# Kernel tuning notes

Hardware: AMD Instinct MI355X
Metric: run time of the kernel (lower is better)

The kernel has to match this reference:

```python
import jax, jax.numpy as jnp
import numpy as np

N, E, F_IN, H, MH, C, G = 100000, 3200000, 128, 32, 64, 10, 64

def _seg_sum(data, ids, num):
    return jax.ops.segment_sum(data, ids, num_segments=num)

def gcn_conv(x, row, col, ew, W, b, n):
    # PyG GCNConv: linear first, then self-loops + symmetric edge-weight norm + scatter-add
    h = x @ W  # [N, H]
    loop = jnp.arange(n)
    r = jnp.concatenate([row, loop])
    c = jnp.concatenate([col, loop])
    w = jnp.concatenate([ew, jnp.ones((n,), dtype=ew.dtype)])
    deg = _seg_sum(w, c, n)
    dinv = jnp.where(deg > 0, jax.lax.rsqrt(deg), 0.0)
    norm = dinv[r] * w * dinv[c]  # [E+N]
    out = _seg_sum(norm[:, None] * h[r], c, n)  # scatter to targets
    return out + b

def setup_inputs():
    key = jax.random.key(0)
    ks = jax.random.split(key, 16)
    inp = {
        "x": jax.random.normal(ks[0], (N, F_IN), dtype=jnp.float32),
        "edge_index": jax.random.randint(ks[1], (2, E), 0, N, dtype=jnp.int64),
        "edge_weight": jax.random.uniform(ks[2], (E,), dtype=jnp.float32),
        "batch": jnp.sort(jax.random.randint(ks[3], (N,), 0, G, dtype=jnp.int64)),
    }
    def lin(k, i, o):
        s = 1.0 / np.sqrt(i)
        k1, k2 = jax.random.split(k)
        return (jax.random.uniform(k1, (i, o), minval=-s, maxval=s, dtype=jnp.float32),
                jax.random.uniform(k2, (o,), minval=-s, maxval=s, dtype=jnp.float32))
    inp["W1"], inp["b1"] = lin(ks[4], F_IN, H)
    inp["W2"], inp["b2"] = lin(ks[5], H, H)
    inp["W3"], inp["b3"] = lin(ks[6], H, H)
    inp["Wm0"], inp["bm0"] = lin(ks[7], H, MH)
    inp["Wm1"], inp["bm1"] = lin(ks[8], MH, MH)
    inp["Wout"], inp["bout"] = lin(ks[9], MH, C)
    return inp

def reference(x, edge_index, edge_weight, batch, W1, b1, W2, b2, W3, b3, Wm0, bm0, Wm1, bm1, Wout, bout):
    row, col = edge_index[0], edge_index[1]
    h = jax.nn.relu(gcn_conv(x, row, col, edge_weight, W1, b1, N))
    h = jax.nn.relu(gcn_conv(h, row, col, edge_weight, W2, b2, N))
    h = gcn_conv(h, row, col, edge_weight, W3, b3, N)
    # global mean pool over graphs
    sums = _seg_sum(h, batch, G)
    counts = _seg_sum(jnp.ones((N,), dtype=h.dtype), batch, G)
    g = sums / jnp.maximum(counts, 1.0)[:, None]
    # dropout p=0.5 is identity at inference (training=False)
    g = jax.nn.relu(g @ Wm0 + bm0)
    g = jax.nn.relu(g @ Wm1 + bm1)
    return g @ Wout + bout
```

## Files before the change

kernel.cpp:

```cpp
#include <hip/hip_runtime.h>

#define NN 100000
#define NE 3200000
#define FIN 128
#define HID 32
#define MH  64
#define NC  10
#define NG  64
#define NBKT 782
#define NBLK 512
#define EPB  (NE / NBLK)
#define SCANL (NBKT * NBLK)
#define SRCMASK 0x1FFFF
#define BCAP 5120

typedef float floatx2 __attribute__((ext_vector_type(2)));

__global__ __launch_bounds__(1024)
void hist_bkt(const int* __restrict__ ei, int* __restrict__ cnt2) {
    __shared__ int h[NBKT];
    int tid = threadIdx.x, blk = blockIdx.x;
    for (int b = tid; b < NBKT; b += 1024) h[b] = 0;
    __syncthreads();
    int base = blk * EPB;
    for (int i = tid; i < EPB; i += 1024)
        atomicAdd(&h[ei[NE + base + i] >> 7], 1);
    __syncthreads();
    for (int b = tid; b < NBKT; b += 1024) cnt2[b * NBLK + blk] = h[b];
}

__global__ void scan_block(const int* __restrict__ in, int* __restrict__ out,
                           int* __restrict__ bsum, int n) {
    __shared__ int lds[256];
    int tid = threadIdx.x;
    int base = blockIdx.x * 1024 + tid * 4;
    int v0 = 0, v1 = 0, v2 = 0, v3 = 0;
    if (base + 0 < n) v0 = in[base + 0];
    if (base + 1 < n) v1 = in[base + 1];
    if (base + 2 < n) v2 = in[base + 2];
    if (base + 3 < n) v3 = in[base + 3];
    int s = v0 + v1 + v2 + v3;
    lds[tid] = s;
    __syncthreads();
    for (int off = 1; off < 256; off <<= 1) {
        int val = (tid >= off) ? lds[tid - off] : 0;
        __syncthreads();
        lds[tid] += val;
        __syncthreads();
    }
    int excl = lds[tid] - s;
    if (tid == 255) bsum[blockIdx.x] = lds[255];
    if (base + 0 < n) out[base + 0] = excl;
    if (base + 1 < n) out[base + 1] = excl + v0;
    if (base + 2 < n) out[base + 2] = excl + v0 + v1;
    if (base + 3 < n) out[base + 3] = excl + v0 + v1 + v2;
}

__global__ void scan_top(int* __restrict__ bsum, int nb, float* __restrict__ sc) {
    int lane = threadIdx.x;
    for (int i = lane; i < NG * HID + NG; i += 64) sc[i] = 0.0f;
    int carry = 0;
    for (int base = 0; base < nb; base += 64) {
        int i = base + lane;
        int orig = (i < nb) ? bsum[i] : 0;
        int v = orig;
#pragma unroll
        for (int off = 1; off < 64; off <<= 1) {
            int t = __shfl_up(v, off, 64);
            if (lane >= off) v += t;
        }
        if (i < nb) bsum[i] = carry + v - orig;
        carry += __shfl(v, 63, 64);
    }
}

__global__ __launch_bounds__(1024)
void scatter_bkt(const int* __restrict__ ei, const float* __restrict__ ew,
                 const int* __restrict__ cnt2, const int* __restrict__ scanned,
                 const int* __restrict__ bsum, int2* __restrict__ tre) {
    __shared__ int2 pay[EPB];
    __shared__ int scur[NBKT];
    __shared__ int hexc[NBKT];
    __shared__ int gbase[NBKT];
    int tid = threadIdx.x, blk = blockIdx.x;
    int myh = 0;
    if (tid < NBKT) {
        int idx = tid * NBLK + blk;
        myh = cnt2[idx];
        gbase[tid] = scanned[idx] + bsum[idx >> 10];
        scur[tid] = myh;
    }
    __syncthreads();
    for (int off = 1; off < NBKT; off <<= 1) {
        int v = (tid < NBKT && tid >= off) ? scur[tid - off] : 0;
        __syncthreads();
        if (tid < NBKT) scur[tid] += v;
        __syncthreads();
    }
    if (tid < NBKT) { int ex = scur[tid] - myh; hexc[tid] = ex; scur[tid] = ex; }
    __syncthreads();
    int base = blk * EPB;
    for (int i = tid; i < EPB; i += 1024) {
        int e = base + i;
        int c = ei[NE + e];
        int r = ei[e];
        unsigned int wb = __float_as_uint(ew[e]);
        int b = c >> 7;
        int j = atomicAdd(&scur[b], 1);
        pay[j] = make_int2(r | ((c & 127) << 17) | ((b & 0xFF) << 24),
                           (int)((wb & ~3u) | ((unsigned)b >> 8)));
    }
    __syncthreads();
    for (int j = tid; j < EPB; j += 1024) {
        int2 q = pay[j];
        int b = (int)((((unsigned)q.y & 3u) << 8) | (((unsigned)q.x >> 24) & 0xFFu));
        int pos = gbase[b] + (j - hexc[b]);
        tre[pos] = make_int2(q.x & 0x00FFFFFF, q.y & ~3);
    }
}

__global__ __launch_bounds__(512)
void sort_k(const int2* __restrict__ tre, const int* __restrict__ scanned,
            const int* __restrict__ bsum, unsigned int* __restrict__ srn4,
            int* __restrict__ rowptr, float* __restrict__ dinv) {
    __shared__ int2 ed[BCAP];
    __shared__ int h[128];
    __shared__ float dw[128];
    __shared__ int cur[128];
    int b = blockIdx.x, tid = threadIdx.x;
    int base = scanned[b * NBLK] + bsum[(b * NBLK) >> 10];
    int end = (b == NBKT - 1)
                  ? NE
                  : scanned[(b + 1) * NBLK] + bsum[((b + 1) * NBLK) >> 10];
    int n = end - base;
    bool staged = (n <= BCAP);
    if (tid < 128) { h[tid] = 0; dw[tid] = 0.f; }
    __syncthreads();
    for (int i = tid; i < n; i += 512) {
        int2 q = tre[base + i];
        if (staged) ed[i] = q;
        int key = (q.x >> 17) & 127;
        atomicAdd(&h[key], 1);
        atomicAdd(&dw[key], __int_as_float(q.y));
    }
    __syncthreads();
    if (tid < 64) {
        int lane = tid;
        int carry = 0;
#pragma unroll
        for (int c = 0; c < 2; ++c) {
            int idx = c * 64 + lane;
            int hv = h[idx];
            int v = hv;
#pragma unroll
            for (int off = 1; off < 64; off <<= 1) {
                int t = __shfl_up(v, off, 64);
                if (lane >= off) v += t;
            }
            cur[idx] = base + carry + v - hv;
            int node = b * 128 + idx;
            if (node < NN) {
                rowptr[node] = base + carry + v;
                dinv[node] = rsqrtf(1.0f + dw[idx]);
            }
            carry += __shfl(v, 63, 64);
        }
    }
    __syncthreads();
    for (int i = tid; i < n; i += 512) {
        int2 q = staged ? ed[i] : tre[base + i];
        int key = (q.x >> 17) & 127;
        int pos = atomicAdd(&cur[key], 1);
        unsigned int wb = (unsigned)q.y;
        wb += 0x7FFFu + ((wb >> 16) & 1u);
        srn4[pos] = (unsigned)(q.x & SRCMASK) | (((wb >> 16) & 0x7FFFu) << 17);
    }
}

template <int IN_DIM, bool RELU_IN>
__global__ __launch_bounds__(256)
void linear_k(const float* __restrict__ in, const float* __restrict__ W,
              const float* __restrict__ dinv, unsigned int* __restrict__ tmp8) {
    constexpr int J4 = IN_DIM / 4;
    constexpr int XSS = J4 + 1;
    __shared__ float4 xs[64 * XSS];
    __shared__ float4 wp[IN_DIM * 8];
    int tid = threadIdx.x;
    for (int idx = tid; idx < IN_DIM * 8; idx += 256) {
        int j = idx >> 3, kg = idx & 7;
        const float* wr = W + j * 32 + kg * 4;
        wp[idx] = make_float4(wr[0], wr[1], wr[2], wr[3]);
    }
    int rbase = blockIdx.x * 64;
    const float4* in4 = (const float4*)in;
    for (int idx = tid; idx < 64 * J4; idx += 256) {
        int row = idx / J4, j4 = idx % J4;
        int grow = rbase + row;
        float4 v = (grow < NN) ? in4[(size_t)grow * J4 + j4]
                               : make_float4(0.f, 0.f, 0.f, 0.f);
        if (RELU_IN) {
            v.x = fmaxf(v.x, 0.f); v.y = fmaxf(v.y, 0.f);
            v.z = fmaxf(v.z, 0.f); v.w = fmaxf(v.w, 0.f);
        }
        xs[row * XSS + j4] = v;
    }
    __syncthreads();
    int kg = tid & 7;
    int rp = tid >> 3;
    int r0 = rbase + 2 * rp;
    if (r0 >= NN) return;
    const float4* x0 = &xs[(2 * rp) * XSS];
    const float4* x1 = &xs[(2 * rp + 1) * XSS];
    float a00 = 0, a01 = 0, a02 = 0, a03 = 0;
    float a10 = 0, a11 = 0, a12 = 0, a13 = 0;
#pragma unroll
    for (int j4 = 0; j4 < J4; ++j4) {
        float4 v0 = x0[j4], v1 = x1[j4];
        const float4* wj = &wp[j4 * 4 * 8 + kg];
        float4 w0 = wj[0], w1 = wj[8], w2 = wj[16], w3 = wj[24];
#define LSTEP(VX0, VX1, W4) \
        a00 = fmaf(VX0, W4.x, a00); a01 = fmaf(VX0, W4.y, a01); \
        a02 = fmaf(VX0, W4.z, a02); a03 = fmaf(VX0, W4.w, a03); \
        a10 = fmaf(VX1, W4.x, a10); a11 = fmaf(VX1, W4.y, a11); \
        a12 = fmaf(VX1, W4.z, a12); a13 = fmaf(VX1, W4.w, a13);
        LSTEP(v0.x, v1.x, w0)
        LSTEP(v0.y, v1.y, w1)
        LSTEP(v0.z, v1.z, w2)
        LSTEP(v0.w, v1.w, w3)
#undef LSTEP
    }
    float d0 = dinv[r0], d1 = dinv[r0 + 1];
    a00 *= d0; a01 *= d0; a02 *= d0; a03 *= d0;
    a10 *= d1; a11 *= d1; a12 *= d1; a13 *= d1;
    int q0 = __builtin_amdgcn_cvt_pk_fp8_f32(a00, a01, 0, false);
    q0 = __builtin_amdgcn_cvt_pk_fp8_f32(a02, a03, q0, true);
    int q1 = __builtin_amdgcn_cvt_pk_fp8_f32(a10, a11, 0, false);
    q1 = __builtin_amdgcn_cvt_pk_fp8_f32(a12, a13, q1, true);
    tmp8[r0 * 8 + kg] = (unsigned int)q0;
    tmp8[(r0 + 1) * 8 + kg] = (unsigned int)q1;
}

struct AccR { floatx2 r0, r1, r2, r3, r4, r5, r6, r7; };

#define ACC8(A0,A1,A2,A3,A4,A5,A6,A7, U, W) { \
    floatx2 lo_, hi_; \
    lo_ = __builtin_amdgcn_cvt_pk_f32_fp8(U.x, false); \
    hi_ = __builtin_amdgcn_cvt_pk_f32_fp8(U.x, true); \
    A0 += lo_ * W; A1 += hi_ * W; \
    lo_ = __builtin_amdgcn_cvt_pk_f32_fp8(U.y, false); \
    hi_ = __builtin_amdgcn_cvt_pk_f32_fp8(U.y, true); \
    A2 += lo_ * W; A3 += hi_ * W; \
    lo_ = __builtin_amdgcn_cvt_pk_f32_fp8(U.z, false); \
    hi_ = __builtin_amdgcn_cvt_pk_f32_fp8(U.z, true); \
    A4 += lo_ * W; A5 += hi_ * W; \
    lo_ = __builtin_amdgcn_cvt_pk_f32_fp8(U.w, false); \
    hi_ = __builtin_amdgcn_cvt_pk_f32_fp8(U.w, true); \
    A6 += lo_ * W; A7 += hi_ * W; }

__device__ __forceinline__ AccR agg_core(const unsigned int* __restrict__ srn4,
                                         const int* __restrict__ rowptr,
                                         const unsigned int* __restrict__ tmp8,
                                         int nid, int s, unsigned int cb) {
    const char* t8 = (const char*)tmp8;
    int end = rowptr[nid];
    int start = (nid == 0) ? 0 : rowptr[nid - 1];
    floatx2 a0 = {0.f,0.f}, a1 = {0.f,0.f}, a2 = {0.f,0.f}, a3 = {0.f,0.f};
    floatx2 a4 = {0.f,0.f}, a5 = {0.f,0.f}, a6 = {0.f,0.f}, a7 = {0.f,0.f};
    floatx2 b0 = {0.f,0.f}, b1 = {0.f,0.f}, b2 = {0.f,0.f}, b3 = {0.f,0.f};
    floatx2 b4 = {0.f,0.f}, b5 = {0.f,0.f}, b6 = {0.f,0.f}, b7 = {0.f,0.f};
    int eM = end - 1;
    for (int e = start + s; e < end; e += 32) {
        int i1 = min(e + 8, eM);
        int i2 = min(e + 16, eM);
        int i3 = min(e + 24, eM);
        unsigned int p0 = srn4[e];
        unsigned int p1 = srn4[i1];
        unsigned int p2 = srn4[i2];
        unsigned int p3 = srn4[i3];
        uint4 u0 = *(const uint4*)(t8 + (((p0 & SRCMASK) << 5) | cb));
        uint4 u1 = *(const uint4*)(t8 + (((p1 & SRCMASK) << 5) | cb));
        uint4 u2 = *(const uint4*)(t8 + (((p2 & SRCMASK) << 5) | cb));
        uint4 u3 = *(const uint4*)(t8 + (((p3 & SRCMASK) << 5) | cb));
        float w0 = __uint_as_float((p0 >> 1) & 0x7FFF0000u);
        float w1 = (e + 8  <= eM) ? __uint_as_float((p1 >> 1) & 0x7FFF0000u) : 0.f;
        float w2 = (e + 16 <= eM) ? __uint_as_float((p2 >> 1) & 0x7FFF0000u) : 0.f;
        float w3 = (e + 24 <= eM) ? __uint_as_float((p3 >> 1) & 0x7FFF0000u) : 0.f;
        ACC8(a0,a1,a2,a3,a4,a5,a6,a7, u0, w0)
        ACC8(b0,b1,b2,b3,b4,b5,b6,b7, u1, w1)
        ACC8(a0,a1,a2,a3,a4,a5,a6,a7, u2, w2)
        ACC8(b0,b1,b2,b3,b4,b5,b6,b7, u3, w3)
    }
    a0 += b0; a1 += b1; a2 += b2; a3 += b3;
    a4 += b4; a5 += b5; a6 += b6; a7 += b7;
#define REDM(M) { \
    a0.x += __shfl_xor(a0.x, M, 64); a0.y += __shfl_xor(a0.y, M, 64); \
    a1.x += __shfl_xor(a1.x, M, 64); a1.y += __shfl_xor(a1.y, M, 64); \
    a2.x += __shfl_xor(a2.x, M, 64); a2.y += __shfl_xor(a2.y, M, 64); \
    a3.x += __shfl_xor(a3.x, M, 64); a3.y += __shfl_xor(a3.y, M, 64); \
    a4.x += __shfl_xor(a4.x, M, 64); a4.y += __shfl_xor(a4.y, M, 64); \
    a5.x += __shfl_xor(a5.x, M, 64); a5.y += __shfl_xor(a5.y, M, 64); \
    a6.x += __shfl_xor(a6.x, M, 64); a6.y += __shfl_xor(a6.y, M, 64); \
    a7.x += __shfl_xor(a7.x, M, 64); a7.y += __shfl_xor(a7.y, M, 64); }
    REDM(2) REDM(4) REDM(8)
#undef REDM
    AccR r;
    r.r0 = a0; r.r1 = a1; r.r2 = a2; r.r3 = a3;
    r.r4 = a4; r.r5 = a5; r.r6 = a6; r.r7 = a7;
    return r;
}

#define EPILOGUE16(O0,O1,O2,O3, NID, CB, D, BIAS, A, RELU) { \
    const char* t8_ = (const char*)tmp8; \
    uint4 sv_ = *(const uint4*)(t8_ + (((unsigned)(NID)) << 5) + (CB)); \
    floatx2 s0_ = __builtin_amdgcn_cvt_pk_f32_fp8(sv_.x, false); \
    floatx2 s1_ = __builtin_amdgcn_cvt_pk_f32_fp8(sv_.x, true); \
    floatx2 s2_ = __builtin_amdgcn_cvt_pk_f32_fp8(sv_.y, false); \
    floatx2 s3_ = __builtin_amdgcn_cvt_pk_f32_fp8(sv_.y, true); \
    floatx2 s4_ = __builtin_amdgcn_cvt_pk_f32_fp8(sv_.z, false); \
    floatx2 s5_ = __builtin_amdgcn_cvt_pk_f32_fp8(sv_.z, true); \
    floatx2 s6_ = __builtin_amdgcn_cvt_pk_f32_fp8(sv_.w, false); \
    floatx2 s7_ = __builtin_amdgcn_cvt_pk_f32_fp8(sv_.w, true); \
    const float4* bp_ = (const float4*)(BIAS) + 4 * c; \
    float4 bq0_ = bp_[0], bq1_ = bp_[1], bq2_ = bp_[2], bq3_ = bp_[3]; \
    O0.x = bq0_.x + (D) * (s0_.x + A.r0.x); \
    O0.y = bq0_.y + (D) * (s0_.y + A.r0.y); \
    O0.z = bq0_.z + (D) * (s1_.x + A.r1.x); \
    O0.w = bq0_.w + (D) * (s1_.y + A.r1.y); \
    O1.x = bq1_.x + (D) * (s2_.x + A.r2.x); \
    O1.y = bq1_.y + (D) * (s2_.y + A.r2.y); \
    O1.z = bq1_.z + (D) * (s3_.x + A.r3.x); \
    O1.w = bq1_.w + (D) * (s3_.y + A.r3.y); \
    O2.x = bq2_.x + (D) * (s4_.x + A.r4.x); \
    O2.y = bq2_.y + (D) * (s4_.y + A.r4.y); \
    O2.z = bq2_.z + (D) * (s5_.x + A.r5.x); \
    O2.w = bq2_.w + (D) * (s5_.y + A.r5.y); \
    O3.x = bq3_.x + (D) * (s6_.x + A.r6.x); \
    O3.y = bq3_.y + (D) * (s6_.y + A.r6.y); \
    O3.z = bq3_.z + (D) * (s7_.x + A.r7.x); \
    O3.w = bq3_.w + (D) * (s7_.y + A.r7.y); \
    if (RELU) { \
        O0.x = fmaxf(O0.x, 0.f); O0.y = fmaxf(O0.y, 0.f); \
        O0.z = fmaxf(O0.z, 0.f); O0.w = fmaxf(O0.w, 0.f); \
        O1.x = fmaxf(O1.x, 0.f); O1.y = fmaxf(O1.y, 0.f); \
        O1.z = fmaxf(O1.z, 0.f); O1.w = fmaxf(O1.w, 0.f); \
        O2.x = fmaxf(O2.x, 0.f); O2.y = fmaxf(O2.y, 0.f); \
        O2.z = fmaxf(O2.z, 0.f); O2.w = fmaxf(O2.w, 0.f); \
        O3.x = fmaxf(O3.x, 0.f); O3.y = fmaxf(O3.y, 0.f); \
        O3.z = fmaxf(O3.z, 0.f); O3.w = fmaxf(O3.w, 0.f); \
    } }

__global__ __launch_bounds__(256)
void aggregate(const unsigned int* __restrict__ srn4,
               const int* __restrict__ rowptr,
               const float* __restrict__ dinv,
               const float* __restrict__ bias,
               const unsigned int* __restrict__ tmp8,
               float* __restrict__ h) {
    int tid = threadIdx.x;
    int nid = (blockIdx.x * 256 + tid) >> 4;
    int lane = tid & 63;
    int c = lane & 1, s = (lane >> 1) & 7;
    unsigned int cb = (unsigned int)c * 16u;
    AccR A = agg_core(srn4, rowptr, tmp8, nid, s, cb);
    if ((lane & 14) == 0) {
        float d = dinv[nid];
        float4 o0, o1, o2, o3;
        EPILOGUE16(o0, o1, o2, o3, nid, cb, d, bias, A, false)
        float4* hp = (float4*)(h + (size_t)nid * HID + 16 * c);
        hp[0] = o0; hp[1] = o1; hp[2] = o2; hp[3] = o3;
    }
}

__global__ __launch_bounds__(256)
void agg_lin(const unsigned int* __restrict__ srn4,
             const int* __restrict__ rowptr,
             const float* __restrict__ dinv,
             const float* __restrict__ bias,
             const float* __restrict__ Wn,
             const unsigned int* __restrict__ tmp8,
             unsigned int* __restrict__ tmp8_out) {
    __shared__ float hrow[4][4][HID];
    __shared__ float Wt[32][36];
    int tid = threadIdx.x;
    for (int idx = tid; idx < 1024; idx += 256)
        Wt[idx & 31][idx >> 5] = Wn[idx];
    int nid = (blockIdx.x * 256 + tid) >> 4;
    int wv = tid >> 6;
    int lane = tid & 63;
    int n = (lane >> 4) & 3;
    int c = lane & 1, s = (lane >> 1) & 7;
    unsigned int cb = (unsigned int)c * 16u;
    __syncthreads();
    AccR A = agg_core(srn4, rowptr, tmp8, nid, s, cb);
    float d = dinv[nid];
    if ((lane & 14) == 0) {
        float4 o0, o1, o2, o3;
        EPILOGUE16(o0, o1, o2, o3, nid, cb, d, bias, A, true)
        float4* hp = (float4*)&hrow[wv][n][16 * c];
        hp[0] = o0; hp[1] = o1; hp[2] = o2; hp[3] = o3;
    }
    int j0 = lane & 15;
    const float4* hb = (const float4*)&hrow[wv][n][0];
    float4 h0 = hb[0], h1 = hb[1], h2 = hb[2], h3 = hb[3];
    float4 h4 = hb[4], h5 = hb[5], h6 = hb[6], h7 = hb[7];
    const float4* w0p = (const float4*)&Wt[j0][0];
    const float4* w1p = (const float4*)&Wt[j0 + 16][0];
    float y0 = 0.f, y1 = 0.f;
#define MVSTEP(K, HV) { float4 wa_ = w0p[K]; float4 wb_ = w1p[K]; \
    y0 = fmaf(HV.x, wa_.x, y0); y0 = fmaf(HV.y, wa_.y, y0); \
    y0 = fmaf(HV.z, wa_.z, y0); y0 = fmaf(HV.w, wa_.w, y0); \
    y1 = fmaf(HV.x, wb_.x, y1); y1 = fmaf(HV.y, wb_.y, y1); \
    y1 = fmaf(HV.z, wb_.z, y1); y1 = fmaf(HV.w, wb_.w, y1); }
    MVSTEP(0, h0) MVSTEP(1, h1) MVSTEP(2, h2) MVSTEP(3, h3)
    MVSTEP(4, h4) MVSTEP(5, h5) MVSTEP(6, h6) MVSTEP(7, h7)
#undef MVSTEP
    y0 *= d; y1 *= d;
    float p1 = __shfl_down(y0, 1, 64);
    float p2 = __shfl_down(y0, 2, 64);
    float p3 = __shfl_down(y0, 3, 64);
    float q1 = __shfl_down(y1, 1, 64);
    float q2 = __shfl_down(y1, 2, 64);
    float q3 = __shfl_down(y1, 3, 64);
    if ((j0 & 3) == 0) {
        int t = j0 >> 2;
        int w0 = __builtin_amdgcn_cvt_pk_fp8_f32(y0, p1, 0, false);
        w0 = __builtin_amdgcn_cvt_pk_fp8_f32(p2, p3, w0, true);
        int w1 = __builtin_amdgcn_cvt_pk_fp8_f32(y1, q1, 0, false);
        w1 = __builtin_amdgcn_cvt_pk_fp8_f32(q2, q3, w1, true);
        tmp8_out[nid * 8 + t] = (unsigned int)w0;
        tmp8_out[nid * 8 + 4 + t] = (unsigned int)w1;
    }
}

__global__ void pool_k(const float* __restrict__ h, const int* __restrict__ batch,
                       float* __restrict__ sums, float* __restrict__ counts) {
    int t = blockIdx.x * 256 + threadIdx.x;
    int chunk = t >> 5, k = t & 31;
    int n0 = chunk * 32;
    if (n0 >= NN) return;
    int n1 = min(n0 + 32, NN);
    int g = batch[n0];
    float acc = 0.f, cacc = 0.f;
    for (int i = n0; i < n1; ++i) {
        int gi = batch[i];
        if (gi != g) {
            atomicAdd(&sums[g * HID + k], acc);
            if (k == 0) atomicAdd(&counts[g], cacc);
            g = gi; acc = 0.f; cacc = 0.f;
        }
        acc += h[(size_t)i * HID + k];
        cacc += 1.f;
    }
    atomicAdd(&sums[g * HID + k], acc);
    if (k == 0) atomicAdd(&counts[g], cacc);
}

__global__ __launch_bounds__(64)
void mlp_k(const float* __restrict__ sums, const float* __restrict__ counts,
           const float* __restrict__ Wm0, const float* __restrict__ bm0,
           const float* __restrict__ Wm1, const float* __restrict__ bm1,
           const float* __restrict__ Wout, const float* __restrict__ bout,
           float* __restrict__ out) {
    __shared__ float g0[HID];
    __shared__ float g1[MH];
    __shared__ float g2[MH];
    int g = blockIdx.x;
    int k = threadIdx.x;
    if (k < HID) g0[k] = sums[g * HID + k] / fmaxf(counts[g], 1.0f);
    __syncthreads();
    float acc = bm0[k];
#pragma unroll
    for (int j = 0; j < HID; ++j) acc = fmaf(g0[j], Wm0[j * MH + k], acc);
    g1[k] = fmaxf(acc, 0.f);
    __syncthreads();
    float acc2 = bm1[k];
#pragma unroll
    for (int j = 0; j < MH; ++j) acc2 = fmaf(g1[j], Wm1[j * MH + k], acc2);
    g2[k] = fmaxf(acc2, 0.f);
    __syncthreads();
    if (k < NC) {
        float acc3 = bout[k];
#pragma unroll
        for (int j = 0; j < MH; ++j) acc3 = fmaf(g2[j], Wout[j * NC + k], acc3);
        out[g * NC + k] = acc3;
    }
}

extern "C" void kernel_launch(void* const* d_in, const int* in_sizes, int n_in,
                              void* d_out, int out_size, void* d_ws, size_t ws_size,
                              hipStream_t stream) {
    const float* x    = (const float*)d_in[0];
    const int*   ei   = (const int*)d_in[1];
    const float* ew   = (const float*)d_in[2];
    const int*   batch= (const int*)d_in[3];
    const float* W1   = (const float*)d_in[4];
    const float* b1   = (const float*)d_in[5];
    const float* W2   = (const float*)d_in[6];
    const float* b2   = (const float*)d_in[7];
    const float* W3   = (const float*)d_in[8];
    const float* b3   = (const float*)d_in[9];
    const float* Wm0  = (const float*)d_in[10];
    const float* bm0  = (const float*)d_in[11];
    const float* Wm1  = (const float*)d_in[12];
    const float* bm1  = (const float*)d_in[13];
    const float* Wout = (const float*)d_in[14];
    const float* bout = (const float*)d_in[15];
    float* out = (float*)d_out;

    char* p = (char*)d_ws;
    unsigned int* srn4 = (unsigned int*)p; p += sizeof(unsigned int) * (size_t)NE;
    char*  S   = p;                      p += 12 * (size_t)NE;
    int2*  tre = (int2*)S;
    int*   cnt2    = (int*)(S + sizeof(int2) * (size_t)NE);
    int*   scanned = cnt2 + SCANL;
    unsigned int* tmp8  = (unsigned int*)S;
    unsigned int* tmp8b = tmp8 + (size_t)NN * 8;
    float* hA  = (float*)(S + 2 * (size_t)NN * HID);
    int*   bsum    = (int*)p;            p += sizeof(int) * 512;
    float* dinv    = (float*)p;          p += sizeof(float) * NN;
    int*   rowptr  = (int*)p;            p += sizeof(int) * NN;
    float* sums    = (float*)p;          p += sizeof(float) * NG * HID;
    float* counts  = (float*)p;

    dim3 blk(256);
    const int NB_SCAN = (SCANL + 1023) / 1024;
    const int NB_LIN = (NN + 63) / 64;
    const int NB_AGG = 6250;

    hist_bkt<<<NBLK, 1024, 0, stream>>>(ei, cnt2);
    scan_block<<<NB_SCAN, blk, 0, stream>>>(cnt2, scanned, bsum, SCANL);
    scan_top<<<1, 64, 0, stream>>>(bsum, NB_SCAN, sums);
    scatter_bkt<<<NBLK, 1024, 0, stream>>>(ei, ew, cnt2, scanned, bsum, tre);
    sort_k<<<NBKT, 512, 0, stream>>>(tre, scanned, bsum, srn4, rowptr, dinv);

    linear_k<FIN, false><<<NB_LIN, blk, 0, stream>>>(x, W1, dinv, tmp8);
    agg_lin<<<NB_AGG, blk, 0, stream>>>(srn4, rowptr, dinv, b1, W2, tmp8, tmp8b);
    agg_lin<<<NB_AGG, blk, 0, stream>>>(srn4, rowptr, dinv, b2, W3, tmp8b, tmp8);
    aggregate<<<NB_AGG, blk, 0, stream>>>(srn4, rowptr, dinv, b3, tmp8, hA);

    pool_k<<<391, blk, 0, stream>>>(hA, batch, sums, counts);
    mlp_k<<<NG, 64, 0, stream>>>(sums, counts, Wm0, bm0, Wm1, bm1, Wout, bout, out);
}
```

Baseline: 361.2 us.

## Aggregate with 8 lanes per node, each lane gathering full 32-byte rows

The aggregation kernels now assign 8 lanes per node instead of 16. Each lane loads a whole 32-byte fp8 feature row as two uint4 loads, rather than having two lanes each fetch half a row. This halves the grid and cuts the shuffle reduction width. In agg_lin, every lane computes the full ReLU epilogue and a 4-output matvec slice, which removes the shared-memory staging of the hidden row. The trade-off is higher register pressure from 16 accumulator pairs and fewer waves in flight for latency hiding.

```diff
diff --git a/kernel.cpp b/kernel.cpp
--- a/kernel.cpp
+++ b/kernel.cpp
@@ -240,34 +240,49 @@
     tmp8[(r0 + 1) * 8 + kg] = (unsigned int)q1;
 }
 
-struct AccR { floatx2 r0, r1, r2, r3, r4, r5, r6, r7; };
-
-#define ACC8(A0,A1,A2,A3,A4,A5,A6,A7, U, W) { \
+struct AccR {
+    floatx2 r0, r1, r2, r3, r4, r5, r6, r7;
+    floatx2 r8, r9, r10, r11, r12, r13, r14, r15;
+};
+
+#define ACC16(UL, UH, W) { \
     floatx2 lo_, hi_; \
-    lo_ = __builtin_amdgcn_cvt_pk_f32_fp8(U.x, false); \
-    hi_ = __builtin_amdgcn_cvt_pk_f32_fp8(U.x, true); \
-    A0 += lo_ * W; A1 += hi_ * W; \
-    lo_ = __builtin_amdgcn_cvt_pk_f32_fp8(U.y, false); \
-    hi_ = __builtin_amdgcn_cvt_pk_f32_fp8(U.y, true); \
-    A2 += lo_ * W; A3 += hi_ * W; \
-    lo_ = __builtin_amdgcn_cvt_pk_f32_fp8(U.z, false); \
-    hi_ = __builtin_amdgcn_cvt_pk_f32_fp8(U.z, true); \
-    A4 += lo_ * W; A5 += hi_ * W; \
-    lo_ = __builtin_amdgcn_cvt_pk_f32_fp8(U.w, false); \
-    hi_ = __builtin_amdgcn_cvt_pk_f32_fp8(U.w, true); \
-    A6 += lo_ * W; A7 += hi_ * W; }
+    lo_ = __builtin_amdgcn_cvt_pk_f32_fp8(UL.x, false); \
+    hi_ = __builtin_amdgcn_cvt_pk_f32_fp8(UL.x, true); \
+    a0 += lo_ * W; a1 += hi_ * W; \
+    lo_ = __builtin_amdgcn_cvt_pk_f32_fp8(UL.y, false); \
+    hi_ = __builtin_amdgcn_cvt_pk_f32_fp8(UL.y, true); \
+    a2 += lo_ * W; a3 += hi_ * W; \
+    lo_ = __builtin_amdgcn_cvt_pk_f32_fp8(UL.z, false); \
+    hi_ = __builtin_amdgcn_cvt_pk_f32_fp8(UL.z, true); \
+    a4 += lo_ * W; a5 += hi_ * W; \
+    lo_ = __builtin_amdgcn_cvt_pk_f32_fp8(UL.w, false); \
+    hi_ = __builtin_amdgcn_cvt_pk_f32_fp8(UL.w, true); \
+    a6 += lo_ * W; a7 += hi_ * W; \
+    lo_ = __builtin_amdgcn_cvt_pk_f32_fp8(UH.x, false); \
+    hi_ = __builtin_amdgcn_cvt_pk_f32_fp8(UH.x, true); \
+    a8 += lo_ * W; a9 += hi_ * W; \
+    lo_ = __builtin_amdgcn_cvt_pk_f32_fp8(UH.y, false); \
+    hi_ = __builtin_amdgcn_cvt_pk_f32_fp8(UH.y, true); \
+    a10 += lo_ * W; a11 += hi_ * W; \
+    lo_ = __builtin_amdgcn_cvt_pk_f32_fp8(UH.z, false); \
+    hi_ = __builtin_amdgcn_cvt_pk_f32_fp8(UH.z, true); \
+    a12 += lo_ * W; a13 += hi_ * W; \
+    lo_ = __builtin_amdgcn_cvt_pk_f32_fp8(UH.w, false); \
+    hi_ = __builtin_amdgcn_cvt_pk_f32_fp8(UH.w, true); \
+    a14 += lo_ * W; a15 += hi_ * W; }
 
 __device__ __forceinline__ AccR agg_core(const unsigned int* __restrict__ srn4,
                                          const int* __restrict__ rowptr,
                                          const unsigned int* __restrict__ tmp8,
-                                         int nid, int s, unsigned int cb) {
+                                         int nid, int s) {
     const char* t8 = (const char*)tmp8;
     int end = rowptr[nid];
     int start = (nid == 0) ? 0 : rowptr[nid - 1];
     floatx2 a0 = {0.f,0.f}, a1 = {0.f,0.f}, a2 = {0.f,0.f}, a3 = {0.f,0.f};
     floatx2 a4 = {0.f,0.f}, a5 = {0.f,0.f}, a6 = {0.f,0.f}, a7 = {0.f,0.f};
-    floatx2 b0 = {0.f,0.f}, b1 = {0.f,0.f}, b2 = {0.f,0.f}, b3 = {0.f,0.f};
-    floatx2 b4 = {0.f,0.f}, b5 = {0.f,0.f}, b6 = {0.f,0.f}, b7 = {0.f,0.f};
+    floatx2 a8 = {0.f,0.f}, a9 = {0.f,0.f}, a10 = {0.f,0.f}, a11 = {0.f,0.f};
+    floatx2 a12 = {0.f,0.f}, a13 = {0.f,0.f}, a14 = {0.f,0.f}, a15 = {0.f,0.f};
     int eM = end - 1;
     for (int e = start + s; e < end; e += 32) {
         int i1 = min(e + 8, eM);
@@ -277,67 +292,76 @@
         unsigned int p1 = srn4[i1];
         unsigned int p2 = srn4[i2];
         unsigned int p3 = srn4[i3];
-        uint4 u0 = *(const uint4*)(t8 + (((p0 & SRCMASK) << 5) | cb));
-        uint4 u1 = *(const uint4*)(t8 + (((p1 & SRCMASK) << 5) | cb));
-        uint4 u2 = *(const uint4*)(t8 + (((p2 & SRCMASK) << 5) | cb));
-        uint4 u3 = *(const uint4*)(t8 + (((p3 & SRCMASK) << 5) | cb));
+        const char* r0p = t8 + ((p0 & SRCMASK) << 5);
+        const char* r1p = t8 + ((p1 & SRCMASK) << 5);
+        const char* r2p = t8 + ((p2 & SRCMASK) << 5);
+        const char* r3p = t8 + ((p3 & SRCMASK) << 5);
+        uint4 uL0 = *(const uint4*)r0p, uH0 = *(const uint4*)(r0p + 16);
+        uint4 uL1 = *(const uint4*)r1p, uH1 = *(const uint4*)(r1p + 16);
+        uint4 uL2 = *(const uint4*)r2p, uH2 = *(const uint4*)(r2p + 16);
+        uint4 uL3 = *(const uint4*)r3p, uH3 = *(const uint4*)(r3p + 16);
         float w0 = __uint_as_float((p0 >> 1) & 0x7FFF0000u);
         float w1 = (e + 8  <= eM) ? __uint_as_float((p1 >> 1) & 0x7FFF0000u) : 0.f;
         float w2 = (e + 16 <= eM) ? __uint_as_float((p2 >> 1) & 0x7FFF0000u) : 0.f;
         float w3 = (e + 24 <= eM) ? __uint_as_float((p3 >> 1) & 0x7FFF0000u) : 0.f;
-        ACC8(a0,a1,a2,a3,a4,a5,a6,a7, u0, w0)
-        ACC8(b0,b1,b2,b3,b4,b5,b6,b7, u1, w1)
-        ACC8(a0,a1,a2,a3,a4,a5,a6,a7, u2, w2)
-        ACC8(b0,b1,b2,b3,b4,b5,b6,b7, u3, w3)
-    }
-    a0 += b0; a1 += b1; a2 += b2; a3 += b3;
-    a4 += b4; a5 += b5; a6 += b6; a7 += b7;
+        ACC16(uL0, uH0, w0)
+        ACC16(uL1, uH1, w1)
+        ACC16(uL2, uH2, w2)
+        ACC16(uL3, uH3, w3)
+    }
 #define REDM(M) { \
-    a0.x += __shfl_xor(a0.x, M, 64); a0.y += __shfl_xor(a0.y, M, 64); \
-    a1.x += __shfl_xor(a1.x, M, 64); a1.y += __shfl_xor(a1.y, M, 64); \
-    a2.x += __shfl_xor(a2.x, M, 64); a2.y += __shfl_xor(a2.y, M, 64); \
-    a3.x += __shfl_xor(a3.x, M, 64); a3.y += __shfl_xor(a3.y, M, 64); \
-    a4.x += __shfl_xor(a4.x, M, 64); a4.y += __shfl_xor(a4.y, M, 64); \
-    a5.x += __shfl_xor(a5.x, M, 64); a5.y += __shfl_xor(a5.y, M, 64); \
-    a6.x += __shfl_xor(a6.x, M, 64); a6.y += __shfl_xor(a6.y, M, 64); \
-    a7.x += __shfl_xor(a7.x, M, 64); a7.y += __shfl_xor(a7.y, M, 64); }
-    REDM(2) REDM(4) REDM(8)
+    a0.x += __shfl_xor(a0.x, M, 64);  a0.y += __shfl_xor(a0.y, M, 64); \
+    a1.x += __shfl_xor(a1.x, M, 64);  a1.y += __shfl_xor(a1.y, M, 64); \
+    a2.x += __shfl_xor(a2.x, M, 64);  a2.y += __shfl_xor(a2.y, M, 64); \
+    a3.x += __shfl_xor(a3.x, M, 64);  a3.y += __shfl_xor(a3.y, M, 64); \
+    a4.x += __shfl_xor(a4.x, M, 64);  a4.y += __shfl_xor(a4.y, M, 64); \
+    a5.x += __shfl_xor(a5.x, M, 64);  a5.y += __shfl_xor(a5.y, M, 64); \
+    a6.x += __shfl_xor(a6.x, M, 64);  a6.y += __shfl_xor(a6.y, M, 64); \
+    a7.x += __shfl_xor(a7.x, M, 64);  a7.y += __shfl_xor(a7.y, M, 64); \
+    a8.x += __shfl_xor(a8.x, M, 64);  a8.y += __shfl_xor(a8.y, M, 64); \
+    a9.x += __shfl_xor(a9.x, M, 64);  a9.y += __shfl_xor(a9.y, M, 64); \
+    a10.x += __shfl_xor(a10.x, M, 64); a10.y += __shfl_xor(a10.y, M, 64); \
+    a11.x += __shfl_xor(a11.x, M, 64); a11.y += __shfl_xor(a11.y, M, 64); \
+    a12.x += __shfl_xor(a12.x, M, 64); a12.y += __shfl_xor(a12.y, M, 64); \
+    a13.x += __shfl_xor(a13.x, M, 64); a13.y += __shfl_xor(a13.y, M, 64); \
+    a14.x += __shfl_xor(a14.x, M, 64); a14.y += __shfl_xor(a14.y, M, 64); \
+    a15.x += __shfl_xor(a15.x, M, 64); a15.y += __shfl_xor(a15.y, M, 64); }
+    REDM(1) REDM(2) REDM(4)
 #undef REDM
     AccR r;
-    r.r0 = a0; r.r1 = a1; r.r2 = a2; r.r3 = a3;
-    r.r4 = a4; r.r5 = a5; r.r6 = a6; r.r7 = a7;
+    r.r0 = a0;  r.r1 = a1;  r.r2 = a2;  r.r3 = a3;
+    r.r4 = a4;  r.r5 = a5;  r.r6 = a6;  r.r7 = a7;
+    r.r8 = a8;  r.r9 = a9;  r.r10 = a10; r.r11 = a11;
+    r.r12 = a12; r.r13 = a13; r.r14 = a14; r.r15 = a15;
     return r;
 }
 
-#define EPILOGUE16(O0,O1,O2,O3, NID, CB, D, BIAS, A, RELU) { \
-    const char* t8_ = (const char*)tmp8; \
-    uint4 sv_ = *(const uint4*)(t8_ + (((unsigned)(NID)) << 5) + (CB)); \
-    floatx2 s0_ = __builtin_amdgcn_cvt_pk_f32_fp8(sv_.x, false); \
-    floatx2 s1_ = __builtin_amdgcn_cvt_pk_f32_fp8(sv_.x, true); \
-    floatx2 s2_ = __builtin_amdgcn_cvt_pk_f32_fp8(sv_.y, false); \
-    floatx2 s3_ = __builtin_amdgcn_cvt_pk_f32_fp8(sv_.y, true); \
-    floatx2 s4_ = __builtin_amdgcn_cvt_pk_f32_fp8(sv_.z, false); \
-    floatx2 s5_ = __builtin_amdgcn_cvt_pk_f32_fp8(sv_.z, true); \
-    floatx2 s6_ = __builtin_amdgcn_cvt_pk_f32_fp8(sv_.w, false); \
-    floatx2 s7_ = __builtin_amdgcn_cvt_pk_f32_fp8(sv_.w, true); \
-    const float4* bp_ = (const float4*)(BIAS) + 4 * c; \
-    float4 bq0_ = bp_[0], bq1_ = bp_[1], bq2_ = bp_[2], bq3_ = bp_[3]; \
-    O0.x = bq0_.x + (D) * (s0_.x + A.r0.x); \
-    O0.y = bq0_.y + (D) * (s0_.y + A.r0.y); \
-    O0.z = bq0_.z + (D) * (s1_.x + A.r1.x); \
-    O0.w = bq0_.w + (D) * (s1_.y + A.r1.y); \
-    O1.x = bq1_.x + (D) * (s2_.x + A.r2.x); \
-    O1.y = bq1_.y + (D) * (s2_.y + A.r2.y); \
-    O1.z = bq1_.z + (D) * (s3_.x + A.r3.x); \
-    O1.w = bq1_.w + (D) * (s3_.y + A.r3.y); \
-    O2.x = bq2_.x + (D) * (s4_.x + A.r4.x); \
-    O2.y = bq2_.y + (D) * (s4_.y + A.r4.y); \
-    O2.z = bq2_.z + (D) * (s5_.x + A.r5.x); \
-    O2.w = bq2_.w + (D) * (s5_.y + A.r5.y); \
-    O3.x = bq3_.x + (D) * (s6_.x + A.r6.x); \
-    O3.y = bq3_.y + (D) * (s6_.y + A.r6.y); \
-    O3.z = bq3_.z + (D) * (s7_.x + A.r7.x); \
-    O3.w = bq3_.w + (D) * (s7_.y + A.r7.y); \
+#define EPI16(O0,O1,O2,O3, R0,R1,R2,R3,R4,R5,R6,R7, SV, BP, D, RELU) { \
+    floatx2 s0_ = __builtin_amdgcn_cvt_pk_f32_fp8(SV.x, false); \
+    floatx2 s1_ = __builtin_amdgcn_cvt_pk_f32_fp8(SV.x, true); \
+    floatx2 s2_ = __builtin_amdgcn_cvt_pk_f32_fp8(SV.y, false); \
+    floatx2 s3_ = __builtin_amdgcn_cvt_pk_f32_fp8(SV.y, true); \
+    floatx2 s4_ = __builtin_amdgcn_cvt_pk_f32_fp8(SV.z, false); \
+    floatx2 s5_ = __builtin_amdgcn_cvt_pk_f32_fp8(SV.z, true); \
+    floatx2 s6_ = __builtin_amdgcn_cvt_pk_f32_fp8(SV.w, false); \
+    floatx2 s7_ = __builtin_amdgcn_cvt_pk_f32_fp8(SV.w, true); \
+    float4 b0_ = BP[0], b1_ = BP[1], b2_ = BP[2], b3_ = BP[3]; \
+    O0.x = b0_.x + (D) * (s0_.x + R0.x); \
+    O0.y = b0_.y + (D) * (s0_.y + R0.y); \
+    O0.z = b0_.z + (D) * (s1_.x + R1.x); \
+    O0.w = b0_.w + (D) * (s1_.y + R1.y); \
+    O1.x = b1_.x + (D) * (s2_.x + R2.x); \
+    O1.y = b1_.y + (D) * (s2_.y + R2.y); \
+    O1.z = b1_.z + (D) * (s3_.x + R3.x); \
+    O1.w = b1_.w + (D) * (s3_.y + R3.y); \
+    O2.x = b2_.x + (D) * (s4_.x + R4.x); \
+    O2.y = b2_.y + (D) * (s4_.y + R4.y); \
+    O2.z = b2_.z + (D) * (s5_.x + R5.x); \
+    O2.w = b2_.w + (D) * (s5_.y + R5.y); \
+    O3.x = b3_.x + (D) * (s6_.x + R6.x); \
+    O3.y = b3_.y + (D) * (s6_.y + R6.y); \
+    O3.z = b3_.z + (D) * (s7_.x + R7.x); \
+    O3.w = b3_.w + (D) * (s7_.y + R7.y); \
     if (RELU) { \
         O0.x = fmaxf(O0.x, 0.f); O0.y = fmaxf(O0.y, 0.f); \
         O0.z = fmaxf(O0.z, 0.f); O0.w = fmaxf(O0.w, 0.f); \
@@ -357,16 +381,24 @@
                const unsigned int* __restrict__ tmp8,
                float* __restrict__ h) {
     int tid = threadIdx.x;
-    int nid = (blockIdx.x * 256 + tid) >> 4;
+    int nid = (blockIdx.x * 256 + tid) >> 3;
     int lane = tid & 63;
-    int c = lane & 1, s = (lane >> 1) & 7;
-    unsigned int cb = (unsigned int)c * 16u;
-    AccR A = agg_core(srn4, rowptr, tmp8, nid, s, cb);
-    if ((lane & 14) == 0) {
+    int s = lane & 7;
+    AccR A = agg_core(srn4, rowptr, tmp8, nid, s);
+    if (s < 2) {
+        const char* t8 = (const char*)tmp8;
         float d = dinv[nid];
+        uint4 sv = *(const uint4*)(t8 + (((unsigned)nid) << 5) + 16 * s);
+        const float4* bp = (const float4*)bias + 4 * s;
         float4 o0, o1, o2, o3;
-        EPILOGUE16(o0, o1, o2, o3, nid, cb, d, bias, A, false)
-        float4* hp = (float4*)(h + (size_t)nid * HID + 16 * c);
+        if (s == 0) {
+            EPI16(o0, o1, o2, o3, A.r0, A.r1, A.r2, A.r3, A.r4, A.r5, A.r6, A.r7,
+                  sv, bp, d, false)
+        } else {
+            EPI16(o0, o1, o2, o3, A.r8, A.r9, A.r10, A.r11, A.r12, A.r13, A.r14,
+                  A.r15, sv, bp, d, false)
+        }
+        float4* hp = (float4*)(h + (size_t)nid * HID + 16 * s);
         hp[0] = o0; hp[1] = o1; hp[2] = o2; hp[3] = o3;
     }
 }
@@ -379,56 +411,67 @@
              const float* __restrict__ Wn,
              const unsigned int* __restrict__ tmp8,
              unsigned int* __restrict__ tmp8_out) {
-    __shared__ float hrow[4][4][HID];
     __shared__ float Wt[32][36];
     int tid = threadIdx.x;
     for (int idx = tid; idx < 1024; idx += 256)
         Wt[idx & 31][idx >> 5] = Wn[idx];
-    int nid = (blockIdx.x * 256 + tid) >> 4;
-    int wv = tid >> 6;
+    int nid = (blockIdx.x * 256 + tid) >> 3;
     int lane = tid & 63;
-    int n = (lane >> 4) & 3;
-    int c = lane & 1, s = (lane >> 1) & 7;
-    unsigned int cb = (unsigned int)c * 16u;
-    __syncthreads();
-    AccR A = agg_core(srn4, rowptr, tmp8, nid, s, cb);
+    int s = lane & 7;
+    __syncthreads();
+    AccR A = agg_core(srn4, rowptr, tmp8, nid, s);
     float d = dinv[nid];
-    if ((lane & 14) == 0) {
-        float4 o0, o1, o2, o3;
-        EPILOGUE16(o0, o1, o2, o3, nid, cb, d, bias, A, true)
-        float4* hp = (float4*)&hrow[wv][n][16 * c];
-        hp[0] = o0; hp[1] = o1; hp[2] = o2; hp[3] = o3;
-    }
-    int j0 = lane & 15;
-    const float4* hb = (const float4*)&hrow[wv][n][0];
-    float4 h0 = hb[0], h1 = hb[1], h2 = hb[2], h3 = hb[3];
-    float4 h4 = hb[4], h5 = hb[5], h6 = hb[6], h7 = hb[7];
-    const float4* w0p = (const float4*)&Wt[j0][0];
-    const float4* w1p = (const float4*)&Wt[j0 + 16][0];
-    float y0 = 0.f, y1 = 0.f;
-#define MVSTEP(K, HV) { float4 wa_ = w0p[K]; float4 wb_ = w1p[K]; \
+    const char* t8 = (const char*)tmp8;
+    uint4 svL = *(const uint4*)(t8 + (((unsigned)nid) << 5));
+    uint4 svH = *(const uint4*)(t8 + (((unsigned)nid) << 5) + 16);
+    const float4* bl = (const float4*)bias;
+    float4 h0, h1, h2, h3, h4, h5, h6, h7;
+    EPI16(h0, h1, h2, h3, A.r0, A.r1, A.r2, A.r3, A.r4, A.r5, A.r6, A.r7,
+          svL, bl, d, true)
+    EPI16(h4, h5, h6, h7, A.r8, A.r9, A.r10, A.r11, A.r12, A.r13, A.r14, A.r15,
+          svH, (bl + 4), d, true)
+    int j0 = s;
+    const float4* wr0 = (const float4*)&Wt[j0][0];
+    const float4* wr1 = (const float4*)&Wt[j0 + 8][0];
+    const float4* wr2 = (const float4*)&Wt[j0 + 16][0];
+    const float4* wr3 = (const float4*)&Wt[j0 + 24][0];
+    float y0 = 0.f, y1 = 0.f, y2 = 0.f, y3 = 0.f;
+#define MV(K, HV) { \
+    float4 wa_ = wr0[K], wb_ = wr1[K], wc_ = wr2[K], wd_ = wr3[K]; \
     y0 = fmaf(HV.x, wa_.x, y0); y0 = fmaf(HV.y, wa_.y, y0); \
     y0 = fmaf(HV.z, wa_.z, y0); y0 = fmaf(HV.w, wa_.w, y0); \
     y1 = fmaf(HV.x, wb_.x, y1); y1 = fmaf(HV.y, wb_.y, y1); \
-    y1 = fmaf(HV.z, wb_.z, y1); y1 = fmaf(HV.w, wb_.w, y1); }
-    MVSTEP(0, h0) MVSTEP(1, h1) MVSTEP(2, h2) MVSTEP(3, h3)
-    MVSTEP(4, h4) MVSTEP(5, h5) MVSTEP(6, h6) MVSTEP(7, h7)
-#undef MVSTEP
-    y0 *= d; y1 *= d;
-    float p1 = __shfl_down(y0, 1, 64);
-    float p2 = __shfl_down(y0, 2, 64);
-    float p3 = __shfl_down(y0, 3, 64);
-    float q1 = __shfl_down(y1, 1, 64);
-    float q2 = __shfl_down(y1, 2, 64);
-    float q3 = __shfl_down(y1, 3, 64);
-    if ((j0 & 3) == 0) {
-        int t = j0 >> 2;
-        int w0 = __builtin_amdgcn_cvt_pk_fp8_f32(y0, p1, 0, false);
-        w0 = __builtin_amdgcn_cvt_pk_fp8_f32(p2, p3, w0, true);
-        int w1 = __builtin_amdgcn_cvt_pk_fp8_f32(y1, q1, 0, false);
-        w1 = __builtin_amdgcn_cvt_pk_fp8_f32(q2, q3, w1, true);
-        tmp8_out[nid * 8 + t] = (unsigned int)w0;
-        tmp8_out[nid * 8 + 4 + t] = (unsigned int)w1;
+    y1 = fmaf(HV.z, wb_.z, y1); y1 = fmaf(HV.w, wb_.w, y1); \
+    y2 = fmaf(HV.x, wc_.x, y2); y2 = fmaf(HV.y, wc_.y, y2); \
+    y2 = fmaf(HV.z, wc_.z, y2); y2 = fmaf(HV.w, wc_.w, y2); \
+    y3 = fmaf(HV.x, wd_.x, y3); y3 = fmaf(HV.y, wd_.y, y3); \
+    y3 = fmaf(HV.z, wd_.z, y3); y3 = fmaf(HV.w, wd_.w, y3); }
+    MV(0, h0) MV(1, h1) MV(2, h2) MV(3, h3)
+    MV(4, h4) MV(5, h5) MV(6, h6) MV(7, h7)
+#undef MV
+    y0 *= d; y1 *= d; y2 *= d; y3 *= d;
+    float p01 = __shfl_down(y0, 1, 64), p02 = __shfl_down(y0, 2, 64),
+          p03 = __shfl_down(y0, 3, 64);
+    float p11 = __shfl_down(y1, 1, 64), p12 = __shfl_down(y1, 2, 64),
+          p13 = __shfl_down(y1, 3, 64);
+    float p21 = __shfl_down(y2, 1, 64), p22 = __shfl_down(y2, 2, 64),
+          p23 = __shfl_down(y2, 3, 64);
+    float p31 = __shfl_down(y3, 1, 64), p32 = __shfl_down(y3, 2, 64),
+          p33 = __shfl_down(y3, 3, 64);
+    if ((s & 3) == 0) {
+        int bb = nid * 8 + (s >> 2);
+        int q0 = __builtin_amdgcn_cvt_pk_fp8_f32(y0, p01, 0, false);
+        q0 = __builtin_amdgcn_cvt_pk_fp8_f32(p02, p03, q0, true);
+        int q1 = __builtin_amdgcn_cvt_pk_fp8_f32(y1, p11, 0, false);
+        q1 = __builtin_amdgcn_cvt_pk_fp8_f32(p12, p13, q1, true);
+        int q2 = __builtin_amdgcn_cvt_pk_fp8_f32(y2, p21, 0, false);
+        q2 = __builtin_amdgcn_cvt_pk_fp8_f32(p22, p23, q2, true);
+        int q3 = __builtin_amdgcn_cvt_pk_fp8_f32(y3, p31, 0, false);
+        q3 = __builtin_amdgcn_cvt_pk_fp8_f32(p32, p33, q3, true);
+        tmp8_out[bb + 0] = (unsigned int)q0;
+        tmp8_out[bb + 2] = (unsigned int)q1;
+        tmp8_out[bb + 4] = (unsigned int)q2;
+        tmp8_out[bb + 6] = (unsigned int)q3;
     }
 }
 
@@ -525,7 +568,7 @@
     dim3 blk(256);
     const int NB_SCAN = (SCANL + 1023) / 1024;
     const int NB_LIN = (NN + 63) / 64;
-    const int NB_AGG = 6250;
+    const int NB_AGG = 3125;
 
     hist_bkt<<<NBLK, 1024, 0, stream>>>(ei, cnt2);
     scan_block<<<NB_SCAN, blk, 0, stream>>>(cnt2, scanned, bsum, SCANL);
```

Result: no change. 361.9 us (+0.2%).
